# Kernel tuning notes

Measured on AMD Instinct MI355X. Metric: run time of the kernel, lower is better.

Reference implementation:

```python
import jax, jax.numpy as jnp
import numpy as np

O, T, DIN, H, DOUT = 50000, 500000, 128, 256, 128


def setup_inputs() -> dict:
    key = jax.random.key(0)
    ks = jax.random.split(key, 12)
    s = 0.05
    return {
        "obj_vecs": jax.random.normal(ks[0], (O, DIN), jnp.float32),
        "pred_vecs": jax.random.normal(ks[1], (T, DIN), jnp.float32),
        "edges": jax.random.randint(ks[2], (T, 2), 0, O, jnp.int64),
        "w1a": jax.random.normal(ks[3], (3 * DIN, H), jnp.float32) * s,
        "b1a": jax.random.normal(ks[4], (H,), jnp.float32) * s,
        "w1b": jax.random.normal(ks[5], (H, 2 * H + DOUT), jnp.float32) * s,
        "b1b": jax.random.normal(ks[6], (2 * H + DOUT,), jnp.float32) * s,
        "w2a": jax.random.normal(ks[7], (H, H), jnp.float32) * s,
        "b2a": jax.random.normal(ks[8], (H,), jnp.float32) * s,
        "w2b": jax.random.normal(ks[9], (H, DOUT), jnp.float32) * s,
        "b2b": jax.random.normal(ks[10], (DOUT,), jnp.float32) * s,
    }


def reference(obj_vecs, pred_vecs, edges, w1a, b1a, w1b, b1b, w2a, b2a, w2b, b2b):
    n_obj = obj_vecs.shape[0]
    h_dim = w2a.shape[0]
    d_out = w2b.shape[1]
    s_idx = edges[:, 0]
    o_idx = edges[:, 1]
    # gather subject/object node features, concat with predicate: [T, 3*Din]
    cur_t = jnp.concatenate([obj_vecs[s_idx], pred_vecs, obj_vecs[o_idx]], axis=1)
    # edge MLP (net1): Linear-ReLU-Linear-ReLU -> [T, 2H + Dout]
    new_t = jax.nn.relu(jax.nn.relu(cur_t @ w1a + b1a) @ w1b + b1b)
    new_s = new_t[:, :h_dim]
    new_p = new_t[:, h_dim:h_dim + d_out]
    new_o = new_t[:, h_dim + d_out:]
    # scatter-add pooling back to nodes, both endpoints
    idx = jnp.concatenate([s_idx, o_idx])
    vals = jnp.concatenate([new_s, new_o], axis=0)
    pooled = jax.ops.segment_sum(vals, idx, num_segments=n_obj)
    # avg pooling: divide by per-node incidence count (clamped to >= 1)
    counts = jax.ops.segment_sum(jnp.ones(idx.shape[0], obj_vecs.dtype), idx,
                                 num_segments=n_obj)
    pooled = pooled / jnp.clip(counts, 1.0)[:, None]
    # node MLP (net2)
    new_obj = jax.nn.relu(jax.nn.relu(pooled @ w2a + b2a) @ w2b + b2b)
    return new_obj, new_p
```

## Files before the change

kernel.cpp:

```cpp
#include <hip/hip_runtime.h>


using f32x4 = __attribute__((ext_vector_type(4))) float;
using s16x8 = __attribute__((ext_vector_type(8))) short;
typedef unsigned short u16x8 __attribute__((ext_vector_type(8)));

#define VMCNT0  asm volatile("s_waitcnt vmcnt(0)" ::: "memory")
#define VMCNT4  asm volatile("s_waitcnt vmcnt(4)" ::: "memory")
#define VMCNT16 asm volatile("s_waitcnt vmcnt(16)" ::: "memory")
#define VMCNT32 asm volatile("s_waitcnt vmcnt(32)" ::: "memory")
#define LGKM0   asm volatile("s_waitcnt lgkmcnt(0)" ::: "memory")
#define BAR     __builtin_amdgcn_s_barrier()
#define SCHEDB  __builtin_amdgcn_sched_barrier(0)

static __device__ __forceinline__ unsigned short f2b(float f) {
    unsigned int u = __float_as_uint(f);
    unsigned int r = (u + 0x7fffu + ((u >> 16) & 1u)) >> 16;
    return (unsigned short)r;
}

static __device__ __forceinline__ float b2f(unsigned short b) {
    return __uint_as_float(((unsigned)b) << 16);
}

static __device__ __forceinline__ unsigned swz(unsigned row, unsigned byteoff) {
    return byteoff ^ ((row & 7u) << 4);
}

static __device__ __forceinline__ void gload_lds16(const unsigned short* g, unsigned short* l) {
    __builtin_amdgcn_global_load_lds(
        (const __attribute__((address_space(1))) unsigned int*)g,
        (__attribute__((address_space(3))) unsigned int*)l,
        16, 0, 0);
}

__global__ void prep_weights(const float* __restrict__ w1a, const float* __restrict__ w1b,
                             const float* __restrict__ w2a, const float* __restrict__ w2b,
                             unsigned short* __restrict__ w1aT, unsigned short* __restrict__ w1bT,
                             unsigned short* __restrict__ w2aT, unsigned short* __restrict__ w2bT) {
    int t = blockIdx.x * blockDim.x + threadIdx.x;
    if (t < 6 * 16384) {
        int kt = t >> 14;
        int rem = t & 16383; int c = rem >> 6, kk = rem & 63;
        unsigned byte = ((unsigned)(c * 128 + kk * 2)) ^ ((c & 7u) << 4);
        *(unsigned short*)((char*)w1aT + (size_t)kt * 32768 + byte) =
            f2b(w1a[(size_t)(kt * 64 + kk) * 256 + c]);
        return;
    }
    t -= 98304;
    if (t < 10 * 16384) {
        int tile = t >> 14; int nc = tile >> 1, kh = tile & 1;
        int rem = t & 16383; int c = rem >> 7, kk = rem & 127;
        unsigned byte = ((unsigned)(c * 256 + kk * 2)) ^ ((c & 7u) << 4);
        *(unsigned short*)((char*)w1bT + (size_t)tile * 32768 + byte) =
            f2b(w1b[(size_t)(kh * 128 + kk) * 640 + nc * 128 + c]);
        return;
    }
    t -= 163840;
    if (t < 65536) { int n = t >> 8, k = t & 255; w2aT[t] = f2b(w2a[k * 256 + n]); return; }
    t -= 65536;
    if (t < 32768) { int n = t >> 8, k = t & 255; w2bT[t] = f2b(w2b[k * 128 + n]); return; }
}

__global__ void count_kernel_i(const int* __restrict__ edges, int* __restrict__ cnt, int T) {
    int e = blockIdx.x * blockDim.x + threadIdx.x;
    if (e < T) {
        atomicAdd(&cnt[edges[2 * (long long)e]], 1);
        atomicAdd(&cnt[edges[2 * (long long)e + 1]], 1);
    }
}

__global__ void scan_kernel(const int* __restrict__ cnt, int* __restrict__ rowptr,
                            int* __restrict__ cursor, int O) {
    __shared__ int sc[1024];
    const int tid = threadIdx.x;
    const int per = (O + 1023) >> 10;
    const int base = tid * per;
    int s = 0;
    for (int i = 0; i < per; ++i) { int j = base + i; if (j < O) s += cnt[j]; }
    sc[tid] = s;
    __syncthreads();
    for (int d = 1; d < 1024; d <<= 1) {
        int v = (tid >= d) ? sc[tid - d] : 0;
        __syncthreads();
        sc[tid] += v;
        __syncthreads();
    }
    int off = sc[tid] - s;
    for (int i = 0; i < per; ++i) {
        int j = base + i;
        if (j < O) { rowptr[j] = off; cursor[j] = off; off += cnt[j]; }
    }
    if (tid == 0) rowptr[O] = sc[1023];
}

__global__ void fill_kernel(const int* __restrict__ edges, int* __restrict__ cursor,
                            int* __restrict__ csr, int T) {
    int e = blockIdx.x * blockDim.x + threadIdx.x;
    if (e < T) {
        int s = edges[2 * (long long)e];
        int o = edges[2 * (long long)e + 1];
        int ps = atomicAdd(&cursor[s], 1); csr[ps] = e;
        int po = atomicAdd(&cursor[o], 1); csr[po] = T + e;
    }
}

__global__ __launch_bounds__(512, 2) void edge_mlp(
    const float* __restrict__ obj, const float* __restrict__ pred,
    const int* __restrict__ edges,
    const unsigned short* __restrict__ w1aT, const float* __restrict__ b1a,
    const unsigned short* __restrict__ w1bT, const float* __restrict__ b1b,
    unsigned short* __restrict__ edgeout, float* __restrict__ outP, int T) {
    const int m0 = blockIdx.x * 128;
    const int tid = threadIdx.x;
    const int lane = tid & 63, wid = tid >> 6;
    const int wm = wid >> 2, wn = wid & 3;
    const bool evenL = ((lane & 1) == 0);

    __shared__ unsigned short U[65536];
    char* const ldsb = (char*)U;
    unsigned short* const abuf0 = (unsigned short*)(ldsb);
    unsigned short* const abuf1 = (unsigned short*)(ldsb + 16384);
    unsigned short* const Hbuf  = (unsigned short*)(ldsb);
    unsigned short* const bbuf0 = (unsigned short*)(ldsb + 65536);
    unsigned short* const bbuf1 = (unsigned short*)(ldsb + 98304);

    bool okR[4][4];
    #pragma unroll
    for (int mi = 0; mi < 4; ++mi)
        #pragma unroll
        for (int rr = 0; rr < 4; ++rr)
            okR[mi][rr] = (m0 + wm * 64 + mi * 16 + ((lane >> 4) << 2) + rr) < T;

    const int r = tid >> 2;
    const int q = tid & 3;
    int e_r = m0 + r; if (e_r >= T) e_r = T - 1;
    const int sIdx_r = edges[2 * (long long)e_r];
    const int oIdx_r = edges[2 * (long long)e_r + 1];

    float bias1[4], bias2[5][2];
    #pragma unroll
    for (int nj = 0; nj < 4; ++nj) bias1[nj] = b1a[wn * 64 + nj * 16 + (lane & 15)];
    #pragma unroll
    for (int nc = 0; nc < 5; ++nc)
        #pragma unroll
        for (int nj = 0; nj < 2; ++nj)
            bias2[nc][nj] = b1b[nc * 128 + wn * 32 + nj * 16 + (lane & 15)];

    auto aSrc = [&](int kt) -> const float4* {
        const float* s;
        if (kt < 2)      s = obj  + (long long)sIdx_r * 128 + kt * 64;
        else if (kt < 4) s = pred + (long long)e_r   * 128 + (kt - 2) * 64;
        else             s = obj  + (long long)oIdx_r * 128 + (kt - 4) * 64;
        return (const float4*)s;
    };

    auto stageB = [&](const unsigned short* gt, unsigned short* bb) {
        #pragma unroll
        for (int rr4 = 0; rr4 < 4; ++rr4) {
            unsigned off = wid * 4096u + rr4 * 1024u;
            gload_lds16((const unsigned short*)((const char*)gt + off + lane * 16u),
                        (unsigned short*)((char*)bb + off));
        }
    };

    auto writeA = [&](const float4* ap, unsigned short* ab) {
        #pragma unroll
        for (int i = 0; i < 4; ++i) {
            float4 v = ap[i];
            ushort4 pk; pk.x = f2b(v.x); pk.y = f2b(v.y); pk.z = f2b(v.z); pk.w = f2b(v.w);
            unsigned byte = (r * 128u + q * 32u + i * 8u) ^ ((r & 7u) << 4);
            *(ushort4*)((char*)ab + byte) = pk;
        }
    };

    f32x4 acc1[4][4];
    #pragma unroll
    for (int a = 0; a < 4; ++a)
        #pragma unroll
        for (int b = 0; b < 4; ++b) acc1[a][b] = f32x4{0.f, 0.f, 0.f, 0.f};

    auto mfma1 = [&](const unsigned short* ab, const unsigned short* bb) {
        #pragma unroll
        for (int ks = 0; ks < 2; ++ks) {
            const unsigned kk = ks * 32u + ((lane >> 4) << 3);
            s16x8 af[4];
            #pragma unroll
            for (int mi = 0; mi < 4; ++mi) {
                unsigned row = wm * 64u + mi * 16u + (lane & 15);
                af[mi] = *(const s16x8*)((const char*)ab + ((row * 128u + kk * 2u) ^ ((row & 7u) << 4)));
            }
            #pragma unroll
            for (int nj = 0; nj < 4; ++nj) {
                unsigned c = wn * 64u + nj * 16u + (lane & 15);
                s16x8 bf = *(const s16x8*)((const char*)bb + ((c * 128u + kk * 2u) ^ ((c & 7u) << 4)));
                #pragma unroll
                for (int mi = 0; mi < 4; ++mi)
                    acc1[mi][nj] = __builtin_amdgcn_mfma_f32_16x16x32_bf16(af[mi], bf, acc1[mi][nj], 0, 0, 0);
            }
        }
    };

    float4 ap[4];
    {
        const float4* s4 = aSrc(0);
        #pragma unroll
        for (int i = 0; i < 4; ++i) ap[i] = s4[q * 4 + i];
    }
    writeA(ap, abuf0);
    stageB(w1aT, bbuf0);
    {
        const float4* s4 = aSrc(1);
        #pragma unroll
        for (int i = 0; i < 4; ++i) ap[i] = s4[q * 4 + i];
    }
    VMCNT4;
    LGKM0;
    BAR; SCHEDB;

    #pragma unroll
    for (int kt = 0; kt < 6; ++kt) {
        if (kt < 5) stageB(w1aT + (size_t)(kt + 1) * 16384, ((kt + 1) & 1) ? bbuf1 : bbuf0);
        else        stageB(w1bT, bbuf0);
        __builtin_amdgcn_s_setprio(1);
        mfma1((kt & 1) ? abuf1 : abuf0, (kt & 1) ? bbuf1 : bbuf0);
        __builtin_amdgcn_s_setprio(0);
        if (kt < 5) {
            VMCNT4;
            writeA(ap, ((kt + 1) & 1) ? abuf1 : abuf0);
            if (kt < 4) {
                const float4* s4 = aSrc(kt + 2);
                #pragma unroll
                for (int i = 0; i < 4; ++i) ap[i] = s4[q * 4 + i];
                VMCNT4;
            } else {
                VMCNT0;
            }
            LGKM0;
            BAR; SCHEDB;
        }
    }

    LGKM0;
    BAR; SCHEDB;
    #pragma unroll
    for (int nj = 0; nj < 4; ++nj) {
        #pragma unroll
        for (int mi = 0; mi < 4; ++mi)
            #pragma unroll
            for (int rr = 0; rr < 4; ++rr) {
                unsigned row = wm * 64u + mi * 16u + ((lane >> 4) << 2) + rr;
                unsigned col = wn * 64u + nj * 16u + (lane & 15);
                float v = acc1[mi][nj][rr] + bias1[nj];
                v = v > 0.f ? v : 0.f;
                *(unsigned short*)((char*)Hbuf + swz(row, row * 512u + col * 2u)) = f2b(v);
            }
    }
    LGKM0;
    VMCNT0;
    BAR; SCHEDB;

    #pragma unroll
    for (int nc = 0; nc < 5; ++nc) {
        f32x4 acc2[4][2];
        #pragma unroll
        for (int a = 0; a < 4; ++a)
            #pragma unroll
            for (int b = 0; b < 2; ++b) acc2[a][b] = f32x4{0.f, 0.f, 0.f, 0.f};

        #pragma unroll
        for (int kh = 0; kh < 2; ++kh) {
            const int t10 = nc * 2 + kh;
            if (t10 < 9) stageB(w1bT + (size_t)(t10 + 1) * 16384, ((t10 + 1) & 1) ? bbuf1 : bbuf0);
            const unsigned short* bb = (t10 & 1) ? bbuf1 : bbuf0;
            __builtin_amdgcn_s_setprio(1);
            #pragma unroll
            for (int ks = 0; ks < 4; ++ks) {
                const unsigned kkB = ks * 32u + ((lane >> 4) << 3);
                const unsigned kkH = kh * 128u + kkB;
                s16x8 af[4];
                #pragma unroll
                for (int mi = 0; mi < 4; ++mi) {
                    unsigned row = wm * 64u + mi * 16u + (lane & 15);
                    af[mi] = *(const s16x8*)((const char*)Hbuf + swz(row, row * 512u + kkH * 2u));
                }
                #pragma unroll
                for (int nj = 0; nj < 2; ++nj) {
                    unsigned c = wn * 32u + nj * 16u + (lane & 15);
                    s16x8 bf = *(const s16x8*)((const char*)bb + ((c * 256u + kkB * 2u) ^ ((c & 7u) << 4)));
                    #pragma unroll
                    for (int mi = 0; mi < 4; ++mi)
                        acc2[mi][nj] = __builtin_amdgcn_mfma_f32_16x16x32_bf16(af[mi], bf, acc2[mi][nj], 0, 0, 0);
                }
            }
            __builtin_amdgcn_s_setprio(0);

            if (kh == 0) {
                VMCNT0;
                BAR; SCHEDB;
            }
        }

        if (nc == 2) {
            #pragma unroll
            for (int nj = 0; nj < 2; ++nj) {
                int col = nc * 128 + wn * 32 + nj * 16 + (lane & 15);
                #pragma unroll
                for (int mi = 0; mi < 4; ++mi)
                    #pragma unroll
                    for (int rr = 0; rr < 4; ++rr) {
                        int row = wm * 64 + mi * 16 + ((lane >> 4) << 2) + rr;
                        if (okR[mi][rr]) {
                            float v = acc2[mi][nj][rr] + bias2[nc][nj];
                            v = v > 0.f ? v : 0.f;
                            outP[(long long)(m0 + row) * 128 + (col - 256)] = v;
                        }
                    }
            }
            VMCNT32;
            BAR; SCHEDB;
        } else {
            #pragma unroll
            for (int nj = 0; nj < 2; ++nj) {
                int col = nc * 128 + wn * 32 + nj * 16 + (lane & 15);
                int pc = (nc < 2) ? col : (col - 384);
                int pcb = (lane & 1) ? (pc - 1) : pc;
                #pragma unroll
                for (int mi = 0; mi < 4; ++mi) {
                    float vv[4];
                    #pragma unroll
                    for (int rr = 0; rr < 4; ++rr) {
                        float v = acc2[mi][nj][rr] + bias2[nc][nj];
                        vv[rr] = v > 0.f ? v : 0.f;
                    }
                    float nb0 = __shfl_xor(vv[0], 1);
                    float nb1 = __shfl_xor(vv[1], 1);
                    float nb2 = __shfl_xor(vv[2], 1);
                    float nb3 = __shfl_xor(vv[3], 1);
                    #pragma unroll
                    for (int k = 0; k < 2; ++k) {
                        float lo = evenL ? (k ? vv[1] : vv[0]) : (k ? nb3 : nb2);
                        float hi = evenL ? (k ? nb1 : nb0) : (k ? vv[3] : vv[2]);
                        int rsel = evenL ? k : 2 + k;
                        if (okR[mi][rsel]) {
                            int row = wm * 64 + mi * 16 + ((lane >> 4) << 2) + rsel;
                            size_t e = (size_t)(m0 + row);
                            size_t rid = (nc < 2) ? e : (size_t)T + e;
                            unsigned pk = ((unsigned)f2b(hi) << 16) | f2b(lo);
                            *(unsigned*)(edgeout + rid * 256 + pcb) = pk;
                        }
                    }
                }
            }
            if (nc < 4) {
                VMCNT16;
                BAR; SCHEDB;
            }
        }
    }
}

__global__ __launch_bounds__(256, 4) void pool_gather(
    const unsigned short* __restrict__ edgeout, const int* __restrict__ rowptr,
    const int* __restrict__ csr, unsigned short* __restrict__ pooled, int O) {
    int w = blockIdx.x * 4 + (threadIdx.x >> 6);
    if (w >= O) return;
    const int lane = threadIdx.x & 63;
    const int beg = rowptr[w], end = rowptr[w + 1];
    float ax = 0.f, ay = 0.f, az = 0.f, aw = 0.f;
    float bx = 0.f, by = 0.f, bz = 0.f, bw = 0.f;
    int i = beg;
    for (; i + 3 < end; i += 4) {
        int r0 = csr[i], r1 = csr[i + 1], r2 = csr[i + 2], r3 = csr[i + 3];
        ushort4 v0 = *(const ushort4*)(edgeout + (size_t)r0 * 256 + lane * 4);
        ushort4 v1 = *(const ushort4*)(edgeout + (size_t)r1 * 256 + lane * 4);
        ushort4 v2 = *(const ushort4*)(edgeout + (size_t)r2 * 256 + lane * 4);
        ushort4 v3 = *(const ushort4*)(edgeout + (size_t)r3 * 256 + lane * 4);
        ax += b2f(v0.x); ay += b2f(v0.y); az += b2f(v0.z); aw += b2f(v0.w);
        bx += b2f(v1.x); by += b2f(v1.y); bz += b2f(v1.z); bw += b2f(v1.w);
        ax += b2f(v2.x); ay += b2f(v2.y); az += b2f(v2.z); aw += b2f(v2.w);
        bx += b2f(v3.x); by += b2f(v3.y); bz += b2f(v3.z); bw += b2f(v3.w);
    }
    for (; i < end; ++i) {
        int r0 = csr[i];
        ushort4 v0 = *(const ushort4*)(edgeout + (size_t)r0 * 256 + lane * 4);
        ax += b2f(v0.x); ay += b2f(v0.y); az += b2f(v0.z); aw += b2f(v0.w);
    }
    float inv = 1.f / fmaxf((float)(end - beg), 1.f);
    ushort4 o4;
    o4.x = f2b((ax + bx) * inv); o4.y = f2b((ay + by) * inv);
    o4.z = f2b((az + bz) * inv); o4.w = f2b((aw + bw) * inv);
    *(ushort4*)(pooled + (size_t)w * 256 + lane * 4) = o4;
}

__global__ __launch_bounds__(256, 2) void obj_mlp(
    const unsigned short* __restrict__ pooled,
    const unsigned short* __restrict__ w2aT, const float* __restrict__ b2a,
    const unsigned short* __restrict__ w2bT, const float* __restrict__ b2b,
    float* __restrict__ outObj, int O) {
    const int m0 = blockIdx.x * 64;
    const int tid = threadIdx.x;
    const int lane = tid & 63, wid = tid >> 6;
    const int wm = wid >> 1, wn = wid & 1;

    __shared__ unsigned short Abuf[64 * 256];

    {
        const int r = tid >> 2, q = tid & 3;
        int objc = m0 + r; if (objc >= O) objc = O - 1;
        const u16x8* s8 = (const u16x8*)(pooled + (size_t)objc * 256);
        #pragma unroll
        for (int i = 0; i < 8; ++i) {
            u16x8 v = s8[q * 8 + i];
            unsigned byte = r * 512u + (q * 64u + i * 8u) * 2u;
            *(u16x8*)((char*)Abuf + swz(r, byte)) = v;
        }
    }
    __syncthreads();

    f32x4 acc1[2][2][4];
    #pragma unroll
    for (int a = 0; a < 2; ++a)
        #pragma unroll
        for (int b = 0; b < 2; ++b)
            #pragma unroll
            for (int c = 0; c < 4; ++c) acc1[a][b][c] = f32x4{0.f, 0.f, 0.f, 0.f};
    #pragma unroll
    for (int ks = 0; ks < 8; ++ks) {
        const int klane = ks * 32 + ((lane >> 4) << 3);
        s16x8 af[2];
        #pragma unroll
        for (int mi = 0; mi < 2; ++mi) {
            int row = wm * 32 + mi * 16 + (lane & 15);
            af[mi] = *(const s16x8*)((const char*)Abuf + swz(row, row * 512u + klane * 2u));
        }
        #pragma unroll
        for (int nb = 0; nb < 2; ++nb)
            #pragma unroll
            for (int nj = 0; nj < 4; ++nj) {
                int col = nb * 128 + wn * 64 + nj * 16 + (lane & 15);
                s16x8 bf = *(const s16x8*)(w2aT + (long long)col * 256 + klane);
                #pragma unroll
                for (int mi = 0; mi < 2; ++mi)
                    acc1[nb][mi][nj] = __builtin_amdgcn_mfma_f32_16x16x32_bf16(af[mi], bf, acc1[nb][mi][nj], 0, 0, 0);
            }
    }
    __syncthreads();

    #pragma unroll
    for (int nb = 0; nb < 2; ++nb)
        #pragma unroll
        for (int nj = 0; nj < 4; ++nj) {
            int col = nb * 128 + wn * 64 + nj * 16 + (lane & 15);
            float bias = b2a[col];
            #pragma unroll
            for (int mi = 0; mi < 2; ++mi)
                #pragma unroll
                for (int rr = 0; rr < 4; ++rr) {
                    int row = wm * 32 + mi * 16 + ((lane >> 4) << 2) + rr;
                    float v = acc1[nb][mi][nj][rr] + bias;
                    v = v > 0.f ? v : 0.f;
                    *(unsigned short*)((char*)Abuf + swz(row, row * 512u + col * 2u)) = f2b(v);
                }
        }
    __syncthreads();

    f32x4 acc2[2][4];
    #pragma unroll
    for (int b = 0; b < 2; ++b)
        #pragma unroll
        for (int c = 0; c < 4; ++c) acc2[b][c] = f32x4{0.f, 0.f, 0.f, 0.f};
    #pragma unroll
    for (int ks = 0; ks < 8; ++ks) {
        const int klane = ks * 32 + ((lane >> 4) << 3);
        s16x8 af[2];
        #pragma unroll
        for (int mi = 0; mi < 2; ++mi) {
            int row = wm * 32 + mi * 16 + (lane & 15);
            af[mi] = *(const s16x8*)((const char*)Abuf + swz(row, row * 512u + klane * 2u));
        }
        #pragma unroll
        for (int nj = 0; nj < 4; ++nj) {
            int col = wn * 64 + nj * 16 + (lane & 15);
            s16x8 bf = *(const s16x8*)(w2bT + (long long)col * 256 + klane);
            #pragma unroll
            for (int mi = 0; mi < 2; ++mi)
                acc2[mi][nj] = __builtin_amdgcn_mfma_f32_16x16x32_bf16(af[mi], bf, acc2[mi][nj], 0, 0, 0);
        }
    }

    #pragma unroll
    for (int nj = 0; nj < 4; ++nj) {
        int col = wn * 64 + nj * 16 + (lane & 15);
        float bias = b2b[col];
        #pragma unroll
        for (int mi = 0; mi < 2; ++mi)
            #pragma unroll
            for (int rr = 0; rr < 4; ++rr) {
                int row = wm * 32 + mi * 16 + ((lane >> 4) << 2) + rr;
                int o = m0 + row;
                if (o < O) {
                    float v = acc2[mi][nj][rr] + bias;
                    v = v > 0.f ? v : 0.f;
                    outObj[(long long)o * 128 + col] = v;
                }
            }
    }
}

extern "C" void kernel_launch(void* const* d_in, const int* in_sizes, int n_in,
                              void* d_out, int out_size, void* d_ws, size_t ws_size,
                              hipStream_t stream) {
    const float* obj  = (const float*)d_in[0];
    const float* pred = (const float*)d_in[1];
    const int*   edges = (const int*)d_in[2];
    const float* w1a = (const float*)d_in[3];
    const float* b1a = (const float*)d_in[4];
    const float* w1b = (const float*)d_in[5];
    const float* b1b = (const float*)d_in[6];
    const float* w2a = (const float*)d_in[7];
    const float* b2a = (const float*)d_in[8];
    const float* w2b = (const float*)d_in[9];
    const float* b2b = (const float*)d_in[10];

    const int O = in_sizes[0] / 128;
    const int T = in_sizes[1] / 128;

    auto al = [](size_t x) { return (x + 255) & ~(size_t)255; };
    const size_t szEdgeout = (size_t)2 * T * 256 * 2;
    const size_t szPooled  = (size_t)O * 256 * 2;
    const size_t szCnt     = (size_t)O * 4;
    const size_t szRow     = (size_t)(O + 1) * 4;
    const size_t szCsr     = (size_t)2 * T * 4;

    size_t off = 0;
    char* ws = (char*)d_ws;
    unsigned short* edgeout = (unsigned short*)(ws + off); off += al(szEdgeout);
    unsigned short* pooled  = (unsigned short*)(ws + off); off += al(szPooled);
    int* cnt    = (int*)(ws + off); off += al(szCnt);
    int* cursor = (int*)(ws + off); off += al(szCnt);
    int* rowptr = (int*)(ws + off); off += al(szRow);
    int* csr    = (int*)(ws + off); off += al(szCsr);
    unsigned short* w1aT = (unsigned short*)(ws + off); off += (size_t)6 * 16384 * 2;
    unsigned short* w1bT = (unsigned short*)(ws + off); off += (size_t)10 * 16384 * 2;
    unsigned short* w2aT = (unsigned short*)(ws + off); off += (size_t)256 * 256 * 2;
    unsigned short* w2bT = (unsigned short*)(ws + off);

    float* outObj = (float*)d_out;
    float* outP   = (float*)d_out + (size_t)O * 128;

    hipMemsetAsync(cnt, 0, szCnt, stream);
    const int prepElems = 98304 + 163840 + 65536 + 32768;
    prep_weights<<<(prepElems + 255) / 256, 256, 0, stream>>>(w1a, w1b, w2a, w2b, w1aT, w1bT, w2aT, w2bT);
    count_kernel_i<<<(T + 255) / 256, 256, 0, stream>>>(edges, cnt, T);
    scan_kernel<<<1, 1024, 0, stream>>>(cnt, rowptr, cursor, O);
    fill_kernel<<<(T + 255) / 256, 256, 0, stream>>>(edges, cursor, csr, T);
    edge_mlp<<<(T + 127) / 128, 512, 0, stream>>>(obj, pred, edges, w1aT, b1a, w1bT, b1b, edgeout, outP, T);
    pool_gather<<<(O + 3) / 4, 256, 0, stream>>>(edgeout, rowptr, csr, pooled, O);
    obj_mlp<<<(O + 63) / 64, 256, 0, stream>>>(pooled, w2aT, b2a, w2bT, b2b, outObj, O);
}
```

Baseline: 930.7 us.

## Double edge_mlp waves per block and triple-buffer weight tiles in LDS

The edge MLP kernel now launches 16 waves (1024 threads) per 128-edge tile instead of 8, halving each wave's N-slice and accumulator footprint. Weight tiles go into a three-slot LDS ring so each stage is prefetched two steps ahead, and the full vmcnt(0) drains are replaced by partial vmcnt waits. The aim is more latency hiding and finer overlap of weight loads with MFMA work. In exchange, LDS use per block rises to 160KB, which likely allows only one block per CU, and the hand-tuned vmcnt counts must exactly match the outstanding loads to stay correct.

```diff
diff --git a/kernel.cpp b/kernel.cpp
--- a/kernel.cpp
+++ b/kernel.cpp
@@ -5,10 +5,11 @@
 using s16x8 = __attribute__((ext_vector_type(8))) short;
 typedef unsigned short u16x8 __attribute__((ext_vector_type(8)));
 
-#define VMCNT0  asm volatile("s_waitcnt vmcnt(0)" ::: "memory")
+#define VMCNT2  asm volatile("s_waitcnt vmcnt(2)" ::: "memory")
 #define VMCNT4  asm volatile("s_waitcnt vmcnt(4)" ::: "memory")
-#define VMCNT16 asm volatile("s_waitcnt vmcnt(16)" ::: "memory")
-#define VMCNT32 asm volatile("s_waitcnt vmcnt(32)" ::: "memory")
+#define VMCNT8  asm volatile("s_waitcnt vmcnt(8)" ::: "memory")
+#define VMCNT10 asm volatile("s_waitcnt vmcnt(10)" ::: "memory")
+#define VMCNT18 asm volatile("s_waitcnt vmcnt(18)" ::: "memory")
 #define LGKM0   asm volatile("s_waitcnt lgkmcnt(0)" ::: "memory")
 #define BAR     __builtin_amdgcn_s_barrier()
 #define SCHEDB  __builtin_amdgcn_sched_barrier(0)
@@ -105,7 +106,7 @@
     }
 }
 
-__global__ __launch_bounds__(512, 2) void edge_mlp(
+__global__ __launch_bounds__(1024, 4) void edge_mlp(
     const float* __restrict__ obj, const float* __restrict__ pred,
     const int* __restrict__ edges,
     const unsigned short* __restrict__ w1aT, const float* __restrict__ b1a,
@@ -114,16 +115,12 @@
     const int m0 = blockIdx.x * 128;
     const int tid = threadIdx.x;
     const int lane = tid & 63, wid = tid >> 6;
-    const int wm = wid >> 2, wn = wid & 3;
+    const int wm = wid >> 3, wn = wid & 7;
     const bool evenL = ((lane & 1) == 0);
 
-    __shared__ unsigned short U[65536];
+    __shared__ unsigned short U[81920];
     char* const ldsb = (char*)U;
-    unsigned short* const abuf0 = (unsigned short*)(ldsb);
-    unsigned short* const abuf1 = (unsigned short*)(ldsb + 16384);
-    unsigned short* const Hbuf  = (unsigned short*)(ldsb);
-    unsigned short* const bbuf0 = (unsigned short*)(ldsb + 65536);
-    unsigned short* const bbuf1 = (unsigned short*)(ldsb + 98304);
+    char* const bbase = ldsb + 65536;
 
     bool okR[4][4];
     #pragma unroll
@@ -132,55 +129,53 @@
         for (int rr = 0; rr < 4; ++rr)
             okR[mi][rr] = (m0 + wm * 64 + mi * 16 + ((lane >> 4) << 2) + rr) < T;
 
-    const int r = tid >> 2;
-    const int q = tid & 3;
+    const int r = tid >> 3;
+    const int q = tid & 7;
     int e_r = m0 + r; if (e_r >= T) e_r = T - 1;
     const int sIdx_r = edges[2 * (long long)e_r];
     const int oIdx_r = edges[2 * (long long)e_r + 1];
 
-    float bias1[4], bias2[5][2];
-    #pragma unroll
-    for (int nj = 0; nj < 4; ++nj) bias1[nj] = b1a[wn * 64 + nj * 16 + (lane & 15)];
-    #pragma unroll
-    for (int nc = 0; nc < 5; ++nc)
-        #pragma unroll
-        for (int nj = 0; nj < 2; ++nj)
-            bias2[nc][nj] = b1b[nc * 128 + wn * 32 + nj * 16 + (lane & 15)];
-
-    auto aSrc = [&](int kt) -> const float4* {
+    float bias1[2], bias2[5];
+    #pragma unroll
+    for (int nj = 0; nj < 2; ++nj) bias1[nj] = b1a[wn * 32 + nj * 16 + (lane & 15)];
+    #pragma unroll
+    for (int nc = 0; nc < 5; ++nc) bias2[nc] = b1b[nc * 128 + wn * 16 + (lane & 15)];
+
+    auto loadA = [&](int kt, float4* ap) {
         const float* s;
         if (kt < 2)      s = obj  + (long long)sIdx_r * 128 + kt * 64;
         else if (kt < 4) s = pred + (long long)e_r   * 128 + (kt - 2) * 64;
         else             s = obj  + (long long)oIdx_r * 128 + (kt - 4) * 64;
-        return (const float4*)s;
+        const float4* s4 = (const float4*)s;
+        ap[0] = s4[q * 2]; ap[1] = s4[q * 2 + 1];
     };
 
-    auto stageB = [&](const unsigned short* gt, unsigned short* bb) {
-        #pragma unroll
-        for (int rr4 = 0; rr4 < 4; ++rr4) {
-            unsigned off = wid * 4096u + rr4 * 1024u;
+    auto stage32 = [&](const unsigned short* gt, char* bb) {
+        #pragma unroll
+        for (int rr2 = 0; rr2 < 2; ++rr2) {
+            unsigned off = wid * 2048u + rr2 * 1024u;
             gload_lds16((const unsigned short*)((const char*)gt + off + lane * 16u),
-                        (unsigned short*)((char*)bb + off));
+                        (unsigned short*)(bb + off));
         }
     };
 
-    auto writeA = [&](const float4* ap, unsigned short* ab) {
-        #pragma unroll
-        for (int i = 0; i < 4; ++i) {
+    auto writeA = [&](const float4* ap, char* ab) {
+        #pragma unroll
+        for (int i = 0; i < 2; ++i) {
             float4 v = ap[i];
             ushort4 pk; pk.x = f2b(v.x); pk.y = f2b(v.y); pk.z = f2b(v.z); pk.w = f2b(v.w);
-            unsigned byte = (r * 128u + q * 32u + i * 8u) ^ ((r & 7u) << 4);
-            *(ushort4*)((char*)ab + byte) = pk;
+            unsigned byte = (r * 128u + q * 16u + i * 8u) ^ ((r & 7u) << 4);
+            *(ushort4*)(ab + byte) = pk;
         }
     };
 
-    f32x4 acc1[4][4];
+    f32x4 acc1[4][2];
     #pragma unroll
     for (int a = 0; a < 4; ++a)
         #pragma unroll
-        for (int b = 0; b < 4; ++b) acc1[a][b] = f32x4{0.f, 0.f, 0.f, 0.f};
-
-    auto mfma1 = [&](const unsigned short* ab, const unsigned short* bb) {
+        for (int b = 0; b < 2; ++b) acc1[a][b] = f32x4{0.f, 0.f, 0.f, 0.f};
+
+    auto mfma1 = [&](const char* ab, const char* bb) {
         #pragma unroll
         for (int ks = 0; ks < 2; ++ks) {
             const unsigned kk = ks * 32u + ((lane >> 4) << 3);
@@ -188,12 +183,12 @@
             #pragma unroll
             for (int mi = 0; mi < 4; ++mi) {
                 unsigned row = wm * 64u + mi * 16u + (lane & 15);
-                af[mi] = *(const s16x8*)((const char*)ab + ((row * 128u + kk * 2u) ^ ((row & 7u) << 4)));
-            }
-            #pragma unroll
-            for (int nj = 0; nj < 4; ++nj) {
-                unsigned c = wn * 64u + nj * 16u + (lane & 15);
-                s16x8 bf = *(const s16x8*)((const char*)bb + ((c * 128u + kk * 2u) ^ ((c & 7u) << 4)));
+                af[mi] = *(const s16x8*)(ab + ((row * 128u + kk * 2u) ^ ((row & 7u) << 4)));
+            }
+            #pragma unroll
+            for (int nj = 0; nj < 2; ++nj) {
+                unsigned c = wn * 32u + nj * 16u + (lane & 15);
+                s16x8 bf = *(const s16x8*)(bb + ((c * 128u + kk * 2u) ^ ((c & 7u) << 4)));
                 #pragma unroll
                 for (int mi = 0; mi < 4; ++mi)
                     acc1[mi][nj] = __builtin_amdgcn_mfma_f32_16x16x32_bf16(af[mi], bf, acc1[mi][nj], 0, 0, 0);
@@ -201,78 +196,60 @@
         }
     };
 
-    float4 ap[4];
-    {
-        const float4* s4 = aSrc(0);
-        #pragma unroll
-        for (int i = 0; i < 4; ++i) ap[i] = s4[q * 4 + i];
-    }
-    writeA(ap, abuf0);
-    stageB(w1aT, bbuf0);
-    {
-        const float4* s4 = aSrc(1);
-        #pragma unroll
-        for (int i = 0; i < 4; ++i) ap[i] = s4[q * 4 + i];
-    }
+    float4 ap[2];
+    loadA(0, ap);
+    writeA(ap, ldsb);
+    stage32(w1aT, bbase);
+    stage32(w1aT + 16384, bbase + 32768);
+    loadA(1, ap);
     VMCNT4;
     LGKM0;
     BAR; SCHEDB;
 
     #pragma unroll
-    for (int kt = 0; kt < 6; ++kt) {
-        if (kt < 5) stageB(w1aT + (size_t)(kt + 1) * 16384, ((kt + 1) & 1) ? bbuf1 : bbuf0);
-        else        stageB(w1bT, bbuf0);
+    for (int s = 0; s < 6; ++s) {
+        char* const ab = ldsb + (s & 1) * 16384;
+        if (s + 2 < 6) stage32(w1aT + (size_t)(s + 2) * 16384, bbase + ((s + 2) % 3) * 32768);
+        else           stage32(w1bT + (size_t)(s + 2 - 6) * 16384, bbase + ((s + 2) % 3) * 32768);
         __builtin_amdgcn_s_setprio(1);
-        mfma1((kt & 1) ? abuf1 : abuf0, (kt & 1) ? bbuf1 : bbuf0);
+        mfma1(ab, bbase + (s % 3) * 32768);
         __builtin_amdgcn_s_setprio(0);
-        if (kt < 5) {
-            VMCNT4;
-            writeA(ap, ((kt + 1) & 1) ? abuf1 : abuf0);
-            if (kt < 4) {
-                const float4* s4 = aSrc(kt + 2);
-                #pragma unroll
-                for (int i = 0; i < 4; ++i) ap[i] = s4[q * 4 + i];
-                VMCNT4;
-            } else {
-                VMCNT0;
-            }
-            LGKM0;
-            BAR; SCHEDB;
-        }
-    }
-
+        VMCNT2;
+        if (s < 5) {
+            writeA(ap, ldsb + ((s + 1) & 1) * 16384);
+            if (s < 4) loadA(s + 2, ap);
+        }
+        LGKM0;
+        BAR; SCHEDB;
+    }
+
+    #pragma unroll
+    for (int nj = 0; nj < 2; ++nj) {
+        unsigned col = wn * 32u + nj * 16u + (lane & 15);
+        #pragma unroll
+        for (int mi = 0; mi < 4; ++mi)
+            #pragma unroll
+            for (int rr = 0; rr < 4; ++rr) {
+                unsigned row = wm * 64u + mi * 16u + ((lane >> 4) << 2) + rr;
+                float v = acc1[mi][nj][rr] + bias1[nj];
+                v = v > 0.f ? v : 0.f;
+                *(unsigned short*)(ldsb + ((row * 512u + col * 2u) ^ ((row & 7u) << 4))) = f2b(v);
+            }
+    }
     LGKM0;
     BAR; SCHEDB;
-    #pragma unroll
-    for (int nj = 0; nj < 4; ++nj) {
-        #pragma unroll
-        for (int mi = 0; mi < 4; ++mi)
-            #pragma unroll
-            for (int rr = 0; rr < 4; ++rr) {
-                unsigned row = wm * 64u + mi * 16u + ((lane >> 4) << 2) + rr;
-                unsigned col = wn * 64u + nj * 16u + (lane & 15);
-                float v = acc1[mi][nj][rr] + bias1[nj];
-                v = v > 0.f ? v : 0.f;
-                *(unsigned short*)((char*)Hbuf + swz(row, row * 512u + col * 2u)) = f2b(v);
-            }
-    }
-    LGKM0;
-    VMCNT0;
-    BAR; SCHEDB;
 
     #pragma unroll
     for (int nc = 0; nc < 5; ++nc) {
-        f32x4 acc2[4][2];
-        #pragma unroll
-        for (int a = 0; a < 4; ++a)
-            #pragma unroll
-            for (int b = 0; b < 2; ++b) acc2[a][b] = f32x4{0.f, 0.f, 0.f, 0.f};
+        f32x4 acc2[4];
+        #pragma unroll
+        for (int a = 0; a < 4; ++a) acc2[a] = f32x4{0.f, 0.f, 0.f, 0.f};
 
         #pragma unroll
         for (int kh = 0; kh < 2; ++kh) {
-            const int t10 = nc * 2 + kh;
-            if (t10 < 9) stageB(w1bT + (size_t)(t10 + 1) * 16384, ((t10 + 1) & 1) ? bbuf1 : bbuf0);
-            const unsigned short* bb = (t10 & 1) ? bbuf1 : bbuf0;
+            const int s = 6 + nc * 2 + kh;
+            if (s + 2 <= 15) stage32(w1bT + (size_t)(s + 2 - 6) * 16384, bbase + ((s + 2) % 3) * 32768);
+            const char* bb = bbase + (s % 3) * 32768;
             __builtin_amdgcn_s_setprio(1);
             #pragma unroll
             for (int ks = 0; ks < 4; ++ks) {
@@ -282,79 +259,73 @@
                 #pragma unroll
                 for (int mi = 0; mi < 4; ++mi) {
                     unsigned row = wm * 64u + mi * 16u + (lane & 15);
-                    af[mi] = *(const s16x8*)((const char*)Hbuf + swz(row, row * 512u + kkH * 2u));
+                    af[mi] = *(const s16x8*)(ldsb + ((row * 512u + kkH * 2u) ^ ((row & 7u) << 4)));
                 }
-                #pragma unroll
-                for (int nj = 0; nj < 2; ++nj) {
-                    unsigned c = wn * 32u + nj * 16u + (lane & 15);
-                    s16x8 bf = *(const s16x8*)((const char*)bb + ((c * 256u + kkB * 2u) ^ ((c & 7u) << 4)));
-                    #pragma unroll
-                    for (int mi = 0; mi < 4; ++mi)
-                        acc2[mi][nj] = __builtin_amdgcn_mfma_f32_16x16x32_bf16(af[mi], bf, acc2[mi][nj], 0, 0, 0);
+                unsigned c = wn * 16u + (lane & 15);
+                s16x8 bf = *(const s16x8*)(bb + ((c * 256u + kkB * 2u) ^ ((c & 7u) << 4)));
+                #pragma unroll
+                for (int mi = 0; mi < 4; ++mi)
+                    acc2[mi] = __builtin_amdgcn_mfma_f32_16x16x32_bf16(af[mi], bf, acc2[mi], 0, 0, 0);
+            }
+            __builtin_amdgcn_s_setprio(0);
+
+            if (kh == 0) {
+                if (s == 6)       { VMCNT2; }
+                else if (s == 12) { VMCNT18; }
+                else if (s == 14) { VMCNT8; }
+                else              { VMCNT10; }
+                LGKM0; BAR; SCHEDB;
+            }
+        }
+
+        if (nc == 2) {
+            #pragma unroll
+            for (int mi = 0; mi < 4; ++mi)
+                #pragma unroll
+                for (int rr = 0; rr < 4; ++rr) {
+                    int row = wm * 64 + mi * 16 + ((lane >> 4) << 2) + rr;
+                    if (okR[mi][rr]) {
+                        int col = 2 * 128 + wn * 16 + (lane & 15);
+                        float v = acc2[mi][rr] + bias2[2];
+                        v = v > 0.f ? v : 0.f;
+                        outP[(long long)(m0 + row) * 128 + (col - 256)] = v;
+                    }
                 }
-            }
-            __builtin_amdgcn_s_setprio(0);
-
-            if (kh == 0) {
-                VMCNT0;
-                BAR; SCHEDB;
-            }
-        }
-
-        if (nc == 2) {
-            #pragma unroll
-            for (int nj = 0; nj < 2; ++nj) {
-                int col = nc * 128 + wn * 32 + nj * 16 + (lane & 15);
-                #pragma unroll
-                for (int mi = 0; mi < 4; ++mi)
-                    #pragma unroll
-                    for (int rr = 0; rr < 4; ++rr) {
-                        int row = wm * 64 + mi * 16 + ((lane >> 4) << 2) + rr;
-                        if (okR[mi][rr]) {
-                            float v = acc2[mi][nj][rr] + bias2[nc][nj];
-                            v = v > 0.f ? v : 0.f;
-                            outP[(long long)(m0 + row) * 128 + (col - 256)] = v;
-                        }
-                    }
-            }
-            VMCNT32;
-            BAR; SCHEDB;
+            VMCNT18;
+            LGKM0; BAR; SCHEDB;
         } else {
             #pragma unroll
-            for (int nj = 0; nj < 2; ++nj) {
-                int col = nc * 128 + wn * 32 + nj * 16 + (lane & 15);
+            for (int mi = 0; mi < 4; ++mi) {
+                int col = nc * 128 + wn * 16 + (lane & 15);
                 int pc = (nc < 2) ? col : (col - 384);
                 int pcb = (lane & 1) ? (pc - 1) : pc;
-                #pragma unroll
-                for (int mi = 0; mi < 4; ++mi) {
-                    float vv[4];
-                    #pragma unroll
-                    for (int rr = 0; rr < 4; ++rr) {
-                        float v = acc2[mi][nj][rr] + bias2[nc][nj];
-                        vv[rr] = v > 0.f ? v : 0.f;
-                    }
-                    float nb0 = __shfl_xor(vv[0], 1);
-                    float nb1 = __shfl_xor(vv[1], 1);
-                    float nb2 = __shfl_xor(vv[2], 1);
-                    float nb3 = __shfl_xor(vv[3], 1);
-                    #pragma unroll
-                    for (int k = 0; k < 2; ++k) {
-                        float lo = evenL ? (k ? vv[1] : vv[0]) : (k ? nb3 : nb2);
-                        float hi = evenL ? (k ? nb1 : nb0) : (k ? vv[3] : vv[2]);
-                        int rsel = evenL ? k : 2 + k;
-                        if (okR[mi][rsel]) {
-                            int row = wm * 64 + mi * 16 + ((lane >> 4) << 2) + rsel;
-                            size_t e = (size_t)(m0 + row);
-                            size_t rid = (nc < 2) ? e : (size_t)T + e;
-                            unsigned pk = ((unsigned)f2b(hi) << 16) | f2b(lo);
-                            *(unsigned*)(edgeout + rid * 256 + pcb) = pk;
-                        }
+                float vv[4];
+                #pragma unroll
+                for (int rr = 0; rr < 4; ++rr) {
+                    float v = acc2[mi][rr] + bias2[nc];
+                    vv[rr] = v > 0.f ? v : 0.f;
+                }
+                float nb0 = __shfl_xor(vv[0], 1);
+                float nb1 = __shfl_xor(vv[1], 1);
+                float nb2 = __shfl_xor(vv[2], 1);
+                float nb3 = __shfl_xor(vv[3], 1);
+                #pragma unroll
+                for (int k = 0; k < 2; ++k) {
+                    float lo = evenL ? (k ? vv[1] : vv[0]) : (k ? nb3 : nb2);
+                    float hi = evenL ? (k ? nb1 : nb0) : (k ? vv[3] : vv[2]);
+                    int rsel = evenL ? k : 2 + k;
+                    if (okR[mi][rsel]) {
+                        int row = wm * 64 + mi * 16 + ((lane >> 4) << 2) + rsel;
+                        size_t e = (size_t)(m0 + row);
+                        size_t rid = (nc < 2) ? e : (size_t)T + e;
+                        unsigned pk = ((unsigned)f2b(hi) << 16) | f2b(lo);
+                        *(unsigned*)(edgeout + rid * 256 + pcb) = pk;
                     }
                 }
             }
             if (nc < 4) {
-                VMCNT16;
-                BAR; SCHEDB;
+                VMCNT10;
+                LGKM0; BAR; SCHEDB;
             }
         }
     }
@@ -555,7 +526,7 @@
     count_kernel_i<<<(T + 255) / 256, 256, 0, stream>>>(edges, cnt, T);
     scan_kernel<<<1, 1024, 0, stream>>>(cnt, rowptr, cursor, O);
     fill_kernel<<<(T + 255) / 256, 256, 0, stream>>>(edges, cursor, csr, T);
-    edge_mlp<<<(T + 127) / 128, 512, 0, stream>>>(obj, pred, edges, w1aT, b1a, w1bT, b1b, edgeout, outP, T);
+    edge_mlp<<<(T + 127) / 128, 1024, 0, stream>>>(obj, pred, edges, w1aT, b1a, w1bT, b1b, edgeout, outP, T);
     pool_gather<<<(O + 3) / 4, 256, 0, stream>>>(edgeout, rowptr, csr, pooled, O);
     obj_mlp<<<(O + 63) / 64, 256, 0, stream>>>(pooled, w2aT, b2a, w2bT, b2b, outObj, O);
 }
```

Result: slower. 1.143 ms (+22.9%).

## Scatter edge outputs into CSR-sorted slots and triple-buffer weight tiles

Applied to the files above, without the earlier changes.

The fill kernel now records each edge's CSR slot, so edge_mlp writes its subject and object halves straight into node-sorted positions in edgeout. pool_gather can then read contiguous rows without the csr indirection. The weight staging moves from double to triple buffering in LDS (160KB), which deepens the prefetch and uses retuned vmcnt waits. The trade-offs are scattered writes from edge_mlp instead of sequential ones, and higher LDS use that may limit occupancy.

```diff
diff --git a/kernel.cpp b/kernel.cpp
--- a/kernel.cpp
+++ b/kernel.cpp
@@ -5,10 +5,11 @@
 using s16x8 = __attribute__((ext_vector_type(8))) short;
 typedef unsigned short u16x8 __attribute__((ext_vector_type(8)));
 
-#define VMCNT0  asm volatile("s_waitcnt vmcnt(0)" ::: "memory")
 #define VMCNT4  asm volatile("s_waitcnt vmcnt(4)" ::: "memory")
+#define VMCNT8  asm volatile("s_waitcnt vmcnt(8)" ::: "memory")
 #define VMCNT16 asm volatile("s_waitcnt vmcnt(16)" ::: "memory")
-#define VMCNT32 asm volatile("s_waitcnt vmcnt(32)" ::: "memory")
+#define VMCNT20 asm volatile("s_waitcnt vmcnt(20)" ::: "memory")
+#define VMCNT36 asm volatile("s_waitcnt vmcnt(36)" ::: "memory")
 #define LGKM0   asm volatile("s_waitcnt lgkmcnt(0)" ::: "memory")
 #define BAR     __builtin_amdgcn_s_barrier()
 #define SCHEDB  __builtin_amdgcn_sched_barrier(0)
@@ -94,14 +95,14 @@
     if (tid == 0) rowptr[O] = sc[1023];
 }
 
-__global__ void fill_kernel(const int* __restrict__ edges, int* __restrict__ cursor,
-                            int* __restrict__ csr, int T) {
+__global__ void slot_kernel(const int* __restrict__ edges, int* __restrict__ cursor,
+                            int* __restrict__ slotS, int* __restrict__ slotO, int T) {
     int e = blockIdx.x * blockDim.x + threadIdx.x;
     if (e < T) {
         int s = edges[2 * (long long)e];
         int o = edges[2 * (long long)e + 1];
-        int ps = atomicAdd(&cursor[s], 1); csr[ps] = e;
-        int po = atomicAdd(&cursor[o], 1); csr[po] = T + e;
+        slotS[e] = atomicAdd(&cursor[s], 1);
+        slotO[e] = atomicAdd(&cursor[o], 1);
     }
 }
 
@@ -110,6 +111,7 @@
     const int* __restrict__ edges,
     const unsigned short* __restrict__ w1aT, const float* __restrict__ b1a,
     const unsigned short* __restrict__ w1bT, const float* __restrict__ b1b,
+    const int* __restrict__ slotS, const int* __restrict__ slotO,
     unsigned short* __restrict__ edgeout, float* __restrict__ outP, int T) {
     const int m0 = blockIdx.x * 128;
     const int tid = threadIdx.x;
@@ -117,13 +119,9 @@
     const int wm = wid >> 2, wn = wid & 3;
     const bool evenL = ((lane & 1) == 0);
 
-    __shared__ unsigned short U[65536];
+    __shared__ unsigned short U[81920];
     char* const ldsb = (char*)U;
-    unsigned short* const abuf0 = (unsigned short*)(ldsb);
-    unsigned short* const abuf1 = (unsigned short*)(ldsb + 16384);
-    unsigned short* const Hbuf  = (unsigned short*)(ldsb);
-    unsigned short* const bbuf0 = (unsigned short*)(ldsb + 65536);
-    unsigned short* const bbuf1 = (unsigned short*)(ldsb + 98304);
+    char* const bbase = ldsb + 65536;
 
     bool okR[4][4];
     #pragma unroll
@@ -131,6 +129,18 @@
         #pragma unroll
         for (int rr = 0; rr < 4; ++rr)
             okR[mi][rr] = (m0 + wm * 64 + mi * 16 + ((lane >> 4) << 2) + rr) < T;
+
+    int slotSr[4][2], slotOr[4][2];
+    #pragma unroll
+    for (int mi = 0; mi < 4; ++mi)
+        #pragma unroll
+        for (int k = 0; k < 2; ++k) {
+            int rsel = evenL ? k : 2 + k;
+            int e = m0 + wm * 64 + mi * 16 + ((lane >> 4) << 2) + rsel;
+            if (e >= T) e = T - 1;
+            slotSr[mi][k] = slotS[e];
+            slotOr[mi][k] = slotO[e];
+        }
 
     const int r = tid >> 2;
     const int q = tid & 3;
@@ -155,22 +165,26 @@
         return (const float4*)s;
     };
 
-    auto stageB = [&](const unsigned short* gt, unsigned short* bb) {
+    auto tp = [&](int i) -> const unsigned short* {
+        return (i < 6) ? (w1aT + (size_t)i * 16384) : (w1bT + (size_t)(i - 6) * 16384);
+    };
+
+    auto stage32 = [&](const unsigned short* gt, char* bb) {
         #pragma unroll
         for (int rr4 = 0; rr4 < 4; ++rr4) {
             unsigned off = wid * 4096u + rr4 * 1024u;
             gload_lds16((const unsigned short*)((const char*)gt + off + lane * 16u),
-                        (unsigned short*)((char*)bb + off));
+                        (unsigned short*)(bb + off));
         }
     };
 
-    auto writeA = [&](const float4* ap, unsigned short* ab) {
+    auto writeA = [&](const float4* ap, char* ab) {
         #pragma unroll
         for (int i = 0; i < 4; ++i) {
             float4 v = ap[i];
             ushort4 pk; pk.x = f2b(v.x); pk.y = f2b(v.y); pk.z = f2b(v.z); pk.w = f2b(v.w);
             unsigned byte = (r * 128u + q * 32u + i * 8u) ^ ((r & 7u) << 4);
-            *(ushort4*)((char*)ab + byte) = pk;
+            *(ushort4*)(ab + byte) = pk;
         }
     };
 
@@ -180,7 +194,7 @@
         #pragma unroll
         for (int b = 0; b < 4; ++b) acc1[a][b] = f32x4{0.f, 0.f, 0.f, 0.f};
 
-    auto mfma1 = [&](const unsigned short* ab, const unsigned short* bb) {
+    auto mfma1 = [&](const char* ab, const char* bb) {
         #pragma unroll
         for (int ks = 0; ks < 2; ++ks) {
             const unsigned kk = ks * 32u + ((lane >> 4) << 3);
@@ -188,12 +202,12 @@
             #pragma unroll
             for (int mi = 0; mi < 4; ++mi) {
                 unsigned row = wm * 64u + mi * 16u + (lane & 15);
-                af[mi] = *(const s16x8*)((const char*)ab + ((row * 128u + kk * 2u) ^ ((row & 7u) << 4)));
+                af[mi] = *(const s16x8*)(ab + ((row * 128u + kk * 2u) ^ ((row & 7u) << 4)));
             }
             #pragma unroll
             for (int nj = 0; nj < 4; ++nj) {
                 unsigned c = wn * 64u + nj * 16u + (lane & 15);
-                s16x8 bf = *(const s16x8*)((const char*)bb + ((c * 128u + kk * 2u) ^ ((c & 7u) << 4)));
+                s16x8 bf = *(const s16x8*)(bb + ((c * 128u + kk * 2u) ^ ((c & 7u) << 4)));
                 #pragma unroll
                 for (int mi = 0; mi < 4; ++mi)
                     acc1[mi][nj] = __builtin_amdgcn_mfma_f32_16x16x32_bf16(af[mi], bf, acc1[mi][nj], 0, 0, 0);
@@ -207,58 +221,49 @@
         #pragma unroll
         for (int i = 0; i < 4; ++i) ap[i] = s4[q * 4 + i];
     }
-    writeA(ap, abuf0);
-    stageB(w1aT, bbuf0);
+    writeA(ap, ldsb);
+    stage32(tp(0), bbase);
+    stage32(tp(1), bbase + 32768);
     {
         const float4* s4 = aSrc(1);
         #pragma unroll
         for (int i = 0; i < 4; ++i) ap[i] = s4[q * 4 + i];
     }
-    VMCNT4;
-    LGKM0;
-    BAR; SCHEDB;
-
-    #pragma unroll
-    for (int kt = 0; kt < 6; ++kt) {
-        if (kt < 5) stageB(w1aT + (size_t)(kt + 1) * 16384, ((kt + 1) & 1) ? bbuf1 : bbuf0);
-        else        stageB(w1bT, bbuf0);
+    VMCNT8;
+    LGKM0; BAR; SCHEDB;
+
+    #pragma unroll
+    for (int s = 0; s < 6; ++s) {
+        stage32(tp(s + 2), bbase + ((s + 2) % 3) * 32768);
         __builtin_amdgcn_s_setprio(1);
-        mfma1((kt & 1) ? abuf1 : abuf0, (kt & 1) ? bbuf1 : bbuf0);
+        mfma1(ldsb + (s & 1) * 16384, bbase + (s % 3) * 32768);
         __builtin_amdgcn_s_setprio(0);
-        if (kt < 5) {
-            VMCNT4;
-            writeA(ap, ((kt + 1) & 1) ? abuf1 : abuf0);
-            if (kt < 4) {
-                const float4* s4 = aSrc(kt + 2);
+        VMCNT4;
+        if (s < 5) {
+            writeA(ap, ldsb + ((s + 1) & 1) * 16384);
+            if (s < 4) {
+                const float4* s4 = aSrc(s + 2);
                 #pragma unroll
                 for (int i = 0; i < 4; ++i) ap[i] = s4[q * 4 + i];
-                VMCNT4;
-            } else {
-                VMCNT0;
-            }
-            LGKM0;
-            BAR; SCHEDB;
-        }
-    }
-
-    LGKM0;
-    BAR; SCHEDB;
+            }
+        }
+        LGKM0; BAR; SCHEDB;
+    }
+
     #pragma unroll
     for (int nj = 0; nj < 4; ++nj) {
+        unsigned col = wn * 64u + nj * 16u + (lane & 15);
         #pragma unroll
         for (int mi = 0; mi < 4; ++mi)
             #pragma unroll
             for (int rr = 0; rr < 4; ++rr) {
                 unsigned row = wm * 64u + mi * 16u + ((lane >> 4) << 2) + rr;
-                unsigned col = wn * 64u + nj * 16u + (lane & 15);
                 float v = acc1[mi][nj][rr] + bias1[nj];
                 v = v > 0.f ? v : 0.f;
-                *(unsigned short*)((char*)Hbuf + swz(row, row * 512u + col * 2u)) = f2b(v);
-            }
-    }
-    LGKM0;
-    VMCNT0;
-    BAR; SCHEDB;
+                *(unsigned short*)(ldsb + ((row * 512u + col * 2u) ^ ((row & 7u) << 4))) = f2b(v);
+            }
+    }
+    LGKM0; BAR; SCHEDB;
 
     #pragma unroll
     for (int nc = 0; nc < 5; ++nc) {
@@ -270,24 +275,24 @@
 
         #pragma unroll
         for (int kh = 0; kh < 2; ++kh) {
-            const int t10 = nc * 2 + kh;
-            if (t10 < 9) stageB(w1bT + (size_t)(t10 + 1) * 16384, ((t10 + 1) & 1) ? bbuf1 : bbuf0);
-            const unsigned short* bb = (t10 & 1) ? bbuf1 : bbuf0;
+            const int s = 6 + nc * 2 + kh;
+            if (s + 2 <= 15) stage32(tp(s + 2), bbase + ((s + 2) % 3) * 32768);
+            const char* bb = bbase + (s % 3) * 32768;
             __builtin_amdgcn_s_setprio(1);
             #pragma unroll
             for (int ks = 0; ks < 4; ++ks) {
                 const unsigned kkB = ks * 32u + ((lane >> 4) << 3);
-                const unsigned kkH = kh * 128u + kkB;
+                const unsigned kkH = (kh * 128u) + kkB;
                 s16x8 af[4];
                 #pragma unroll
                 for (int mi = 0; mi < 4; ++mi) {
                     unsigned row = wm * 64u + mi * 16u + (lane & 15);
-                    af[mi] = *(const s16x8*)((const char*)Hbuf + swz(row, row * 512u + kkH * 2u));
+                    af[mi] = *(const s16x8*)(ldsb + ((row * 512u + kkH * 2u) ^ ((row & 7u) << 4)));
                 }
                 #pragma unroll
                 for (int nj = 0; nj < 2; ++nj) {
                     unsigned c = wn * 32u + nj * 16u + (lane & 15);
-                    s16x8 bf = *(const s16x8*)((const char*)bb + ((c * 256u + kkB * 2u) ^ ((c & 7u) << 4)));
+                    s16x8 bf = *(const s16x8*)(bb + ((c * 256u + kkB * 2u) ^ ((c & 7u) << 4)));
                     #pragma unroll
                     for (int mi = 0; mi < 4; ++mi)
                         acc2[mi][nj] = __builtin_amdgcn_mfma_f32_16x16x32_bf16(af[mi], bf, acc2[mi][nj], 0, 0, 0);
@@ -296,29 +301,32 @@
             __builtin_amdgcn_s_setprio(0);
 
             if (kh == 0) {
-                VMCNT0;
-                BAR; SCHEDB;
+                if (s == 6)       { VMCNT4; }
+                else if (s == 12) { VMCNT36; }
+                else if (s == 14) { VMCNT16; }
+                else              { VMCNT20; }
+                LGKM0; BAR; SCHEDB;
             }
         }
 
         if (nc == 2) {
             #pragma unroll
             for (int nj = 0; nj < 2; ++nj) {
-                int col = nc * 128 + wn * 32 + nj * 16 + (lane & 15);
+                int col = 2 * 128 + wn * 32 + nj * 16 + (lane & 15);
                 #pragma unroll
                 for (int mi = 0; mi < 4; ++mi)
                     #pragma unroll
                     for (int rr = 0; rr < 4; ++rr) {
                         int row = wm * 64 + mi * 16 + ((lane >> 4) << 2) + rr;
                         if (okR[mi][rr]) {
-                            float v = acc2[mi][nj][rr] + bias2[nc][nj];
+                            float v = acc2[mi][nj][rr] + bias2[2][nj];
                             v = v > 0.f ? v : 0.f;
                             outP[(long long)(m0 + row) * 128 + (col - 256)] = v;
                         }
                     }
             }
-            VMCNT32;
-            BAR; SCHEDB;
+            VMCNT36;
+            LGKM0; BAR; SCHEDB;
         } else {
             #pragma unroll
             for (int nj = 0; nj < 2; ++nj) {
@@ -343,18 +351,16 @@
                         float hi = evenL ? (k ? nb1 : nb0) : (k ? vv[3] : vv[2]);
                         int rsel = evenL ? k : 2 + k;
                         if (okR[mi][rsel]) {
-                            int row = wm * 64 + mi * 16 + ((lane >> 4) << 2) + rsel;
-                            size_t e = (size_t)(m0 + row);
-                            size_t rid = (nc < 2) ? e : (size_t)T + e;
+                            int slot = (nc < 2) ? slotSr[mi][k] : slotOr[mi][k];
                             unsigned pk = ((unsigned)f2b(hi) << 16) | f2b(lo);
-                            *(unsigned*)(edgeout + rid * 256 + pcb) = pk;
+                            *(unsigned*)(edgeout + (size_t)slot * 256 + pcb) = pk;
                         }
                     }
                 }
             }
             if (nc < 4) {
-                VMCNT16;
-                BAR; SCHEDB;
+                VMCNT20;
+                LGKM0; BAR; SCHEDB;
             }
         }
     }
@@ -362,31 +368,31 @@
 
 __global__ __launch_bounds__(256, 4) void pool_gather(
     const unsigned short* __restrict__ edgeout, const int* __restrict__ rowptr,
-    const int* __restrict__ csr, unsigned short* __restrict__ pooled, int O) {
+    unsigned short* __restrict__ pooled, int O) {
     int w = blockIdx.x * 4 + (threadIdx.x >> 6);
     if (w >= O) return;
     const int lane = threadIdx.x & 63;
     const int beg = rowptr[w], end = rowptr[w + 1];
     float ax = 0.f, ay = 0.f, az = 0.f, aw = 0.f;
     float bx = 0.f, by = 0.f, bz = 0.f, bw = 0.f;
-    int i = beg;
-    for (; i + 3 < end; i += 4) {
-        int r0 = csr[i], r1 = csr[i + 1], r2 = csr[i + 2], r3 = csr[i + 3];
-        ushort4 v0 = *(const ushort4*)(edgeout + (size_t)r0 * 256 + lane * 4);
-        ushort4 v1 = *(const ushort4*)(edgeout + (size_t)r1 * 256 + lane * 4);
-        ushort4 v2 = *(const ushort4*)(edgeout + (size_t)r2 * 256 + lane * 4);
-        ushort4 v3 = *(const ushort4*)(edgeout + (size_t)r3 * 256 + lane * 4);
+    const unsigned short* base = edgeout + (size_t)beg * 256 + lane * 4;
+    int n = end - beg;
+    int i = 0;
+    for (; i + 3 < n; i += 4) {
+        ushort4 v0 = *(const ushort4*)(base + (size_t)(i    ) * 256);
+        ushort4 v1 = *(const ushort4*)(base + (size_t)(i + 1) * 256);
+        ushort4 v2 = *(const ushort4*)(base + (size_t)(i + 2) * 256);
+        ushort4 v3 = *(const ushort4*)(base + (size_t)(i + 3) * 256);
         ax += b2f(v0.x); ay += b2f(v0.y); az += b2f(v0.z); aw += b2f(v0.w);
         bx += b2f(v1.x); by += b2f(v1.y); bz += b2f(v1.z); bw += b2f(v1.w);
         ax += b2f(v2.x); ay += b2f(v2.y); az += b2f(v2.z); aw += b2f(v2.w);
         bx += b2f(v3.x); by += b2f(v3.y); bz += b2f(v3.z); bw += b2f(v3.w);
     }
-    for (; i < end; ++i) {
-        int r0 = csr[i];
-        ushort4 v0 = *(const ushort4*)(edgeout + (size_t)r0 * 256 + lane * 4);
+    for (; i < n; ++i) {
+        ushort4 v0 = *(const ushort4*)(base + (size_t)i * 256);
         ax += b2f(v0.x); ay += b2f(v0.y); az += b2f(v0.z); aw += b2f(v0.w);
     }
-    float inv = 1.f / fmaxf((float)(end - beg), 1.f);
+    float inv = 1.f / fmaxf((float)n, 1.f);
     ushort4 o4;
     o4.x = f2b((ax + bx) * inv); o4.y = f2b((ay + by) * inv);
     o4.z = f2b((az + bz) * inv); o4.w = f2b((aw + bw) * inv);
@@ -531,7 +537,7 @@
     const size_t szPooled  = (size_t)O * 256 * 2;
     const size_t szCnt     = (size_t)O * 4;
     const size_t szRow     = (size_t)(O + 1) * 4;
-    const size_t szCsr     = (size_t)2 * T * 4;
+    const size_t szSlot    = (size_t)T * 4;
 
     size_t off = 0;
     char* ws = (char*)d_ws;
@@ -540,7 +546,8 @@
     int* cnt    = (int*)(ws + off); off += al(szCnt);
     int* cursor = (int*)(ws + off); off += al(szCnt);
     int* rowptr = (int*)(ws + off); off += al(szRow);
-    int* csr    = (int*)(ws + off); off += al(szCsr);
+    int* slotS  = (int*)(ws + off); off += al(szSlot);
+    int* slotO  = (int*)(ws + off); off += al(szSlot);
     unsigned short* w1aT = (unsigned short*)(ws + off); off += (size_t)6 * 16384 * 2;
     unsigned short* w1bT = (unsigned short*)(ws + off); off += (size_t)10 * 16384 * 2;
     unsigned short* w2aT = (unsigned short*)(ws + off); off += (size_t)256 * 256 * 2;
@@ -554,8 +561,8 @@
     prep_weights<<<(prepElems + 255) / 256, 256, 0, stream>>>(w1a, w1b, w2a, w2b, w1aT, w1bT, w2aT, w2bT);
     count_kernel_i<<<(T + 255) / 256, 256, 0, stream>>>(edges, cnt, T);
     scan_kernel<<<1, 1024, 0, stream>>>(cnt, rowptr, cursor, O);
-    fill_kernel<<<(T + 255) / 256, 256, 0, stream>>>(edges, cursor, csr, T);
-    edge_mlp<<<(T + 127) / 128, 512, 0, stream>>>(obj, pred, edges, w1aT, b1a, w1bT, b1b, edgeout, outP, T);
-    pool_gather<<<(O + 3) / 4, 256, 0, stream>>>(edgeout, rowptr, csr, pooled, O);
+    slot_kernel<<<(T + 255) / 256, 256, 0, stream>>>(edges, cursor, slotS, slotO, T);
+    edge_mlp<<<(T + 127) / 128, 512, 0, stream>>>(obj, pred, edges, w1aT, b1a, w1bT, b1b, slotS, slotO, edgeout, outP, T);
+    pool_gather<<<(O + 3) / 4, 256, 0, stream>>>(edgeout, rowptr, pooled, O);
     obj_mlp<<<(O + 63) / 64, 256, 0, stream>>>(pooled, w2aT, b2a, w2bT, b2b, outObj, O);
 }
```

New measurement: 917.1 us. About the same (-1.5%).
